# Kernel optimization log

Hardware: AMD Instinct MI355X
Metric: run time of the kernel (lower is better)

The kernel has to match this reference:

```python
import jax, jax.numpy as jnp
import numpy as np

NHEAD, DK, DV, DMODEL, L = 8, 64, 64, 512, 32

def setup_inputs() -> dict:
    key = jax.random.key(0)
    ks = jax.random.split(key, 9)
    B, N = 4, 2048
    s = 1.0 / np.sqrt(DMODEL)
    return {
        "q": jax.random.normal(ks[0], (B, N, DMODEL), jnp.float32),
        "k": jax.random.normal(ks[1], (B, N, DMODEL), jnp.float32),
        "v": jax.random.normal(ks[2], (B, N, DMODEL), jnp.float32),
        "Wq": jax.random.normal(ks[3], (DMODEL, NHEAD * DK), jnp.float32) * s,
        "Wk": jax.random.normal(ks[4], (DMODEL, NHEAD * DK), jnp.float32) * s,
        "Wv": jax.random.normal(ks[5], (DMODEL, NHEAD * DV), jnp.float32) * s,
        "Wfc": jax.random.normal(ks[6], (NHEAD * DV, DMODEL), jnp.float32) * s,
        "ln_g": jnp.ones((DMODEL,), jnp.float32),
        "ln_b": jnp.zeros((DMODEL,), jnp.float32),
    }

def reference(q, k, v, Wq, Wk, Wv, Wfc, ln_g, ln_b):
    B, Nq, _ = q.shape
    residual = q
    # project and split heads: [B, H, N, d]
    qh = (q @ Wq).reshape(B, Nq, NHEAD, DK).transpose(0, 2, 1, 3)
    kh = (k @ Wk).reshape(B, k.shape[1], NHEAD, DK).transpose(0, 2, 1, 3)
    vh = (v @ Wv).reshape(B, v.shape[1], NHEAD, DV).transpose(0, 2, 1, 3)
    # scaled dot-product scores and softmax over keys
    attn = jnp.einsum('bhqd,bhkd->bhqk', qh / jnp.sqrt(jnp.float32(DK)), kh)
    attn = jax.nn.softmax(attn, axis=-1)
    # AWG: keep entries >= l-th largest per row, renormalize
    threshold = jax.lax.top_k(attn, L)[0][..., -1:]  # [B,H,Nq,1]
    W = jnp.where(attn >= threshold, attn, 0.0)
    W_out = W / jnp.sum(W, axis=-1, keepdims=True)
    out = jnp.einsum('bhqk,bhkd->bhqd', W_out, vh)
    out = out.transpose(0, 2, 1, 3).reshape(B, Nq, NHEAD * DV)
    out = out @ Wfc + residual
    # LayerNorm, eps=1e-6
    mu = jnp.mean(out, axis=-1, keepdims=True)
    var = jnp.var(out, axis=-1, keepdims=True)
    return (out - mu) / jnp.sqrt(var + 1e-6) * ln_g + ln_b
```

## Files before the change

### kernel.cpp

```cpp
#include <hip/hip_runtime.h>
#include <hip/hip_fp16.h>

#define BATCH 4
#define NSEQ 2048
#define DMODEL 512
#define NHEAD 8
#define HDIM 64
#define LSEL 32
#define SROWU 2056
#define MAXL 128

typedef __attribute__((ext_vector_type(8))) _Float16 f16x8;
typedef __attribute__((ext_vector_type(4))) float f32x4;

__device__ inline ushort f2h(float x) { __half h = __float2half(x); return *reinterpret_cast<ushort*>(&h); }
__device__ inline uint h2sort(ushort h) { return (h & 0x8000u) ? (uint)(h ^ 0xFFFFu) : (uint)(h | 0x8000u); }
__device__ inline float sort2f(uint su) {
    ushort hb = (su & 0x8000u) ? (ushort)(su ^ 0x8000u) : (ushort)(su ^ 0xFFFFu);
    __half th; *reinterpret_cast<ushort*>(&th) = hb;
    return __half2float(th);
}

__global__ __launch_bounds__(256) void cvtA_kernel(
    const float* __restrict__ q, const float* __restrict__ k, const float* __restrict__ v,
    ushort* __restrict__ q16, ushort* __restrict__ k16, ushort* __restrict__ v16)
{
    const int z = blockIdx.y;
    const float* src = (z == 0) ? q : (z == 1) ? k : v;
    ushort* dst = (z == 0) ? q16 : (z == 1) ? k16 : v16;
    const size_t base = (size_t)blockIdx.x * 2048 + threadIdx.x * 4;
    float4 fa = *(const float4*)(src + base);
    float4 fb = *(const float4*)(src + base + 1024);
    ushort4 ha = {f2h(fa.x), f2h(fa.y), f2h(fa.z), f2h(fa.w)};
    ushort4 hb = {f2h(fb.x), f2h(fb.y), f2h(fb.z), f2h(fb.w)};
    *(ushort4*)(dst + base) = ha;
    *(ushort4*)(dst + base + 1024) = hb;
}

__global__ __launch_bounds__(256) void cvtW_kernel(
    const float* __restrict__ Wq, const float* __restrict__ Wk,
    const float* __restrict__ Wv, const float* __restrict__ Wfc,
    ushort* __restrict__ Wt)
{
    const int z = blockIdx.y;
    const float* W = (z == 0) ? Wq : (z == 1) ? Wk : (z == 2) ? Wv : Wfc;
    ushort* O = Wt + (size_t)z * DMODEL * DMODEL;
    const int gt = blockIdx.x * 256 + threadIdx.x;
    const int n = gt & 511;
    const int kc = (gt >> 9) * 16;
    uint pk[8];
#pragma unroll
    for (int i = 0; i < 8; ++i) {
        uint lo = f2h(W[(size_t)(kc + 2 * i) * DMODEL + n]);
        uint hi = f2h(W[(size_t)(kc + 2 * i + 1) * DMODEL + n]);
        pk[i] = lo | (hi << 16);
    }
    uint4 u0 = {pk[0], pk[1], pk[2], pk[3]};
    uint4 u1 = {pk[4], pk[5], pk[6], pk[7]};
    *(uint4*)(O + (size_t)n * DMODEL + kc) = u0;
    *(uint4*)(O + (size_t)n * DMODEL + kc + 8) = u1;
}

template<int MODE>
__global__ __launch_bounds__(256, 2) void hgemm_kernel(
    const ushort* __restrict__ A0, const ushort* __restrict__ A1, const ushort* __restrict__ A2,
    const ushort* __restrict__ Wt,
    ushort* __restrict__ O0, ushort* __restrict__ O1, ushort* __restrict__ O2,
    float* __restrict__ Ofc)
{
    __shared__ ushort Ah[64][40];
    __shared__ ushort Bh[512][40];

    const int tid = threadIdx.x;
    const int wave = tid >> 6, lane = tid & 63;
    const int lr = lane & 15, lg = lane >> 4;
    const int bm = blockIdx.x * 64;
    const int z = blockIdx.y;

    const ushort* A16 = (MODE == 0) ? (z == 0 ? A0 : z == 1 ? A1 : A2) : A0;
    const ushort* Wz = Wt + (size_t)((MODE == 0) ? z : 3) * (DMODEL * DMODEL);

    f32x4 acc[4][8];
#pragma unroll
    for (int i = 0; i < 4; ++i)
#pragma unroll
        for (int j = 0; j < 8; ++j) acc[i][j] = (f32x4){0.f, 0.f, 0.f, 0.f};

    const int sar = tid >> 2, sak = (tid & 3) * 8;

    for (int k0 = 0; k0 < DMODEL; k0 += 32) {
        __syncthreads();
        *(uint4*)&Ah[sar][sak] = *(const uint4*)(A16 + (size_t)(bm + sar) * DMODEL + k0 + sak);
#pragma unroll
        for (int i = 0; i < 8; ++i) {
            int n = sar + 64 * i;
            *(uint4*)&Bh[n][sak] = *(const uint4*)(Wz + (size_t)n * DMODEL + k0 + sak);
        }
        __syncthreads();
        f16x8 af[4];
#pragma unroll
        for (int fr = 0; fr < 4; ++fr) af[fr] = *(const f16x8*)&Ah[fr * 16 + lr][lg * 8];
#pragma unroll
        for (int fc2 = 0; fc2 < 8; ++fc2) {
            f16x8 bf = *(const f16x8*)&Bh[wave * 128 + fc2 * 16 + lr][lg * 8];
#pragma unroll
            for (int fr = 0; fr < 4; ++fr)
                acc[fr][fc2] = __builtin_amdgcn_mfma_f32_16x16x32_f16(af[fr], bf, acc[fr][fc2], 0, 0, 0);
        }
    }

    if (MODE == 1) {
#pragma unroll
        for (int fr = 0; fr < 4; ++fr)
#pragma unroll
            for (int fc2 = 0; fc2 < 8; ++fc2)
#pragma unroll
                for (int r = 0; r < 4; ++r)
                    Ofc[(size_t)(bm + fr * 16 + lg * 4 + r) * DMODEL + wave * 128 + fc2 * 16 + lr] = acc[fr][fc2][r];
        return;
    }

    ushort* O = (z == 0) ? O0 : (z == 1) ? O1 : O2;
    const int b = bm >> 11;
    const int nseq0 = bm & (NSEQ - 1);
    ushort* smw = (ushort*)&Bh[0][0] + wave * (64 * 72);
#pragma unroll
    for (int hp = 0; hp < 2; ++hp) {
        __syncthreads();
#pragma unroll
        for (int f4 = 0; f4 < 4; ++f4) {
            int fc2 = hp * 4 + f4;
            int nl = f4 * 16 + lr;
#pragma unroll
            for (int fr = 0; fr < 4; ++fr)
#pragma unroll
                for (int r = 0; r < 4; ++r)
                    smw[(fr * 16 + lg * 4 + r) * 72 + nl] = f2h(acc[fr][fc2][r]);
        }
        __syncthreads();
        const int h = wave * 2 + hp;
        ushort* obase = O + ((size_t)(b * NHEAD + h) * NSEQ + nseq0) * HDIM;
#pragma unroll
        for (int i = 0; i < 8; ++i) {
            int m = i * 8 + (lane >> 3);
            int dc = (lane & 7) * 8;
            *(uint4*)(obase + (size_t)m * HDIM + dc) = *(const uint4*)(smw + m * 72 + dc);
        }
    }
}

__device__ inline int wave_sum6(int c) {
    int tot = (int)__popcll(__ballot(c & 1));
    tot += (int)__popcll(__ballot(c & 2)) << 1;
    tot += (int)__popcll(__ballot(c & 4)) << 2;
    tot += (int)__popcll(__ballot(c & 8)) << 3;
    tot += (int)__popcll(__ballot(c & 16)) << 4;
    tot += (int)__popcll(__ballot(c & 32)) << 5;
    return tot;
}

__device__ uint full_thr(const ushort* Sr, int lane, uint lo0) {
    uint flo = lo0, fhi = 0xFFFFu;
    for (int it2 = 0; it2 < 16; ++it2) {
        uint mid = (flo + fhi + 1) >> 1, M = mid << 16;
        int cl = 0;
#pragma unroll
        for (int it = 0; it < 4; ++it) {
            uint4 r4 = *(const uint4*)(Sr + it * 512 + lane * 8);
            cl += ((r4.x << 16) >= M) + ((r4.x & 0xFFFF0000u) >= M);
            cl += ((r4.y << 16) >= M) + ((r4.y & 0xFFFF0000u) >= M);
            cl += ((r4.z << 16) >= M) + ((r4.z & 0xFFFF0000u) >= M);
            cl += ((r4.w << 16) >= M) + ((r4.w & 0xFFFF0000u) >= M);
        }
        bool ge = wave_sum6(cl) >= LSEL;
        flo = ge ? mid : flo;
        fhi = ge ? fhi : mid - 1;
    }
    return flo;
}

__device__ int recount(const ushort* Sr, int lane, uint th) {
    int cs = 0;
#pragma unroll
    for (int it = 0; it < 4; ++it) {
        uint4 r4 = *(const uint4*)(Sr + it * 512 + lane * 8);
        cs += ((r4.x << 16) >= th) + ((r4.x & 0xFFFF0000u) >= th);
        cs += ((r4.y << 16) >= th) + ((r4.y & 0xFFFF0000u) >= th);
        cs += ((r4.z << 16) >= th) + ((r4.z & 0xFFFF0000u) >= th);
        cs += ((r4.w << 16) >= th) + ((r4.w & 0xFFFF0000u) >= th);
    }
    return cs;
}

__device__ float extract_row(const ushort* Sr, int lane, uint th, float Mv,
                             int csel, int pre, ushort* li, float* lwp,
                             uint t0, uint t1, uint t2, uint t3)
{
    const float L2E = 1.4426950408889634f;
    float wp = 0.f;
    bool big = __any(csel > 4);
    if (!big) {
        uint tt0 = t0, tt1 = t1, tt2 = t2, tt3 = t3;
#pragma unroll
        for (int i = 0; i < 4; ++i) {
            uint t = (i == 0) ? tt0 : (i == 1) ? tt1 : (i == 2) ? tt2 : tt3;
            if (t >= th) {
                int pos = pre + i;
                float w = exp2f((sort2f(t >> 16) - Mv) * L2E);
                if (pos < MAXL) { li[pos] = (ushort)(t & 0xFFFFu); lwp[pos] = w; wp += w; }
            }
        }
    } else {
        int pos = pre;
#pragma unroll
        for (int it = 0; it < 4; ++it) {
            uint4 r4 = *(const uint4*)(Sr + it * 512 + lane * 8);
            uint ib = (uint)(it * 512 + lane * 8);
            uint wds[4] = {r4.x, r4.y, r4.z, r4.w};
#pragma unroll
            for (int c = 0; c < 4; ++c) {
                uint vL = wds[c] << 16, vH = wds[c] & 0xFFFF0000u;
                if (vL >= th) {
                    float w = exp2f((sort2f(vL >> 16) - Mv) * L2E);
                    if (pos < MAXL) { li[pos] = (ushort)(ib + c * 2); lwp[pos] = w; wp += w; }
                    ++pos;
                }
                if (vH >= th) {
                    float w = exp2f((sort2f(vH >> 16) - Mv) * L2E);
                    if (pos < MAXL) { li[pos] = (ushort)(ib + c * 2 + 1); lwp[pos] = w; wp += w; }
                    ++pos;
                }
            }
        }
    }
#pragma unroll
    for (int off = 32; off >= 1; off >>= 1) wp += __shfl_xor(wp, off);
    return wp;
}

#define INS(T0, T1, T2, T3, P) { uint m1_ = min(P, T0); T0 = max(P, T0); \
    uint m2_ = min(m1_, T1); T1 = max(m1_, T1); \
    uint m3_ = min(m2_, T2); T2 = max(m2_, T2); T3 = max(m3_, T3); }

__global__ __launch_bounds__(512, 4) void attn_kernel(
    const ushort* __restrict__ qh, const ushort* __restrict__ kh,
    const ushort* __restrict__ vh, ushort* __restrict__ ao)
{
    __shared__ __align__(16) ushort Sbuf[16 * SROWU];
    __shared__ ushort lidx[16][MAXL];
    __shared__ float  lw[16][MAXL];

    const int tid = threadIdx.x;
    const int wave = tid >> 6;
    const int lane = tid & 63;
    const int bh = blockIdx.y;
    const int q0 = blockIdx.x * 16;
    const int lr = lane & 15;
    const int lg = lane >> 4;

    const ushort* Qb = qh + ((size_t)bh * NSEQ + q0) * HDIM;
    const ushort* Kb = kh + (size_t)bh * NSEQ * HDIM;

    f16x8 qf0 = *(const f16x8*)(Qb + lr * HDIM + lg * 8);
    f16x8 qf1 = *(const f16x8*)(Qb + lr * HDIM + 32 + lg * 8);

    for (int t = 0; t < 16; ++t) {
        const int k0 = wave * 256 + t * 16;
        const ushort* Kt = Kb + (size_t)k0 * HDIM;
        f16x8 a0 = *(const f16x8*)(Kt + lr * HDIM + lg * 8);
        f16x8 a1 = *(const f16x8*)(Kt + lr * HDIM + 32 + lg * 8);
        f32x4 acc = {0.f, 0.f, 0.f, 0.f};
        acc = __builtin_amdgcn_mfma_f32_16x16x32_f16(a0, qf0, acc, 0, 0, 0);
        acc = __builtin_amdgcn_mfma_f32_16x16x32_f16(a1, qf1, acc, 0, 0, 0);
        uint2 pk;
        pk.x = h2sort(f2h(acc[0] * 0.125f)) | (h2sort(f2h(acc[1] * 0.125f)) << 16);
        pk.y = h2sort(f2h(acc[2] * 0.125f)) | (h2sort(f2h(acc[3] * 0.125f)) << 16);
        *(uint2*)&Sbuf[lr * SROWU + k0 + lg * 4] = pk;
    }
    __syncthreads();

    const __half* Vb = (const __half*)vh + (size_t)bh * NSEQ * HDIM;
    const int b = bh >> 3, hh = bh & 7;
    const unsigned long long below = (1ULL << lane) - 1ULL;

    const int qrA = wave * 2, qrB = qrA + 1;
    const ushort* SrA = &Sbuf[qrA * SROWU];
    const ushort* SrB = &Sbuf[qrB * SROWU];

    uint tA0 = 0, tA1 = 0, tA2 = 0, tA3 = 0;
    uint tB0 = 0, tB1 = 0, tB2 = 0, tB3 = 0;
#pragma unroll
    for (int it = 0; it < 4; ++it) {
        uint4 a4 = *(const uint4*)(SrA + it * 512 + lane * 8);
        uint4 b4 = *(const uint4*)(SrB + it * 512 + lane * 8);
        uint ib = (uint)(it * 512 + lane * 8);
        uint p;
        p = (a4.x << 16) | (ib + 0); INS(tA0, tA1, tA2, tA3, p);
        p = (a4.x & 0xFFFF0000u) | (ib + 1); INS(tA0, tA1, tA2, tA3, p);
        p = (a4.y << 16) | (ib + 2); INS(tA0, tA1, tA2, tA3, p);
        p = (a4.y & 0xFFFF0000u) | (ib + 3); INS(tA0, tA1, tA2, tA3, p);
        p = (a4.z << 16) | (ib + 4); INS(tA0, tA1, tA2, tA3, p);
        p = (a4.z & 0xFFFF0000u) | (ib + 5); INS(tA0, tA1, tA2, tA3, p);
        p = (a4.w << 16) | (ib + 6); INS(tA0, tA1, tA2, tA3, p);
        p = (a4.w & 0xFFFF0000u) | (ib + 7); INS(tA0, tA1, tA2, tA3, p);
        p = (b4.x << 16) | (ib + 0); INS(tB0, tB1, tB2, tB3, p);
        p = (b4.x & 0xFFFF0000u) | (ib + 1); INS(tB0, tB1, tB2, tB3, p);
        p = (b4.y << 16) | (ib + 2); INS(tB0, tB1, tB2, tB3, p);
        p = (b4.y & 0xFFFF0000u) | (ib + 3); INS(tB0, tB1, tB2, tB3, p);
        p = (b4.z << 16) | (ib + 4); INS(tB0, tB1, tB2, tB3, p);
        p = (b4.z & 0xFFFF0000u) | (ib + 5); INS(tB0, tB1, tB2, tB3, p);
        p = (b4.w << 16) | (ib + 6); INS(tB0, tB1, tB2, tB3, p);
        p = (b4.w & 0xFFFF0000u) | (ib + 7); INS(tB0, tB1, tB2, tB3, p);
    }

    uint mxA = tA0, mxB = tB0;
#pragma unroll
    for (int off = 32; off >= 1; off >>= 1) {
        mxA = max(mxA, (uint)__shfl_xor((int)mxA, off));
        mxB = max(mxB, (uint)__shfl_xor((int)mxB, off));
    }
    const float MvA = sort2f(mxA >> 16), MvB = sort2f(mxB >> 16);

    uint loA = 0, hiA = 0xFFFFu, loB = 0, hiB = 0xFFFFu;
#pragma unroll
    for (int it = 0; it < 16; ++it) {
        uint midA = (loA + hiA + 1) >> 1, MA = midA << 16;
        uint midB = (loB + hiB + 1) >> 1, MB = midB << 16;
        int cA = (tA0 >= MA) + (tA1 >= MA) + (tA2 >= MA) + (tA3 >= MA);
        int cB = (tB0 >= MB) + (tB1 >= MB) + (tB2 >= MB) + (tB3 >= MB);
        int totA = (int)__popcll(__ballot(cA & 1)) + ((int)__popcll(__ballot(cA & 2)) << 1)
                 + ((int)__popcll(__ballot(cA & 4)) << 2);
        int totB = (int)__popcll(__ballot(cB & 1)) + ((int)__popcll(__ballot(cB & 2)) << 1)
                 + ((int)__popcll(__ballot(cB & 4)) << 2);
        bool geA = totA >= LSEL, geB = totB >= LSEL;
        loA = geA ? midA : loA; hiA = geA ? hiA : midA - 1;
        loB = geB ? midB : loB; hiB = geB ? hiB : midB - 1;
    }

    uint thA = loA << 16, thB = loB << 16;
    int cgtA = 0, cselA = 0, cgtB = 0, cselB = 0;
#pragma unroll
    for (int it = 0; it < 4; ++it) {
        uint4 a4 = *(const uint4*)(SrA + it * 512 + lane * 8);
        uint4 b4 = *(const uint4*)(SrB + it * 512 + lane * 8);
#define VC(w, th, cgt, csel) { uint vL_ = (w) << 16, vH_ = (w) & 0xFFFF0000u; \
        cgt += (vL_ > th) + (vH_ > th); csel += (vL_ >= th) + (vH_ >= th); }
        VC(a4.x, thA, cgtA, cselA) VC(a4.y, thA, cgtA, cselA)
        VC(a4.z, thA, cgtA, cselA) VC(a4.w, thA, cgtA, cselA)
        VC(b4.x, thB, cgtB, cselB) VC(b4.y, thB, cgtB, cselB)
        VC(b4.z, thB, cgtB, cselB) VC(b4.w, thB, cgtB, cselB)
#undef VC
    }
    const int CgtA = wave_sum6(cgtA);
    const int CgtB = wave_sum6(cgtB);

    if (CgtA >= LSEL) {
        thA = full_thr(SrA, lane, loA) << 16;
        cselA = recount(SrA, lane, thA);
    }
    if (CgtB >= LSEL) {
        thB = full_thr(SrB, lane, loB) << 16;
        cselB = recount(SrB, lane, thB);
    }

    int preA = 0, totA2 = 0, preB = 0, totB2 = 0;
#pragma unroll
    for (int bb = 0; bb < 6; ++bb) {
        unsigned long long mA = __ballot((cselA >> bb) & 1);
        unsigned long long mB = __ballot((cselB >> bb) & 1);
        preA += (int)__popcll(mA & below) << bb; totA2 += (int)__popcll(mA) << bb;
        preB += (int)__popcll(mB & below) << bb; totB2 += (int)__popcll(mB) << bb;
    }

    float wsumA = extract_row(SrA, lane, thA, MvA, cselA, preA, &lidx[qrA][0], &lw[qrA][0], tA0, tA1, tA2, tA3);
    float wsumB = extract_row(SrB, lane, thB, MvB, cselB, preB, &lidx[qrB][0], &lw[qrB][0], tB0, tB1, tB2, tB3);

    asm volatile("s_waitcnt lgkmcnt(0)" ::: "memory");

    const int nkA = (totA2 < MAXL) ? totA2 : MAXL;
    const int nkB = (totB2 < MAXL) ? totB2 : MAXL;

    float oA = 0.f, oB = 0.f;
    {
        int j = 0;
        for (; j + 4 <= nkA; j += 4) {
            int i0 = lidx[qrA][j + 0]; float w0 = lw[qrA][j + 0];
            int i1 = lidx[qrA][j + 1]; float w1 = lw[qrA][j + 1];
            int i2 = lidx[qrA][j + 2]; float w2 = lw[qrA][j + 2];
            int i3 = lidx[qrA][j + 3]; float w3 = lw[qrA][j + 3];
            oA += w0 * __half2float(Vb[(size_t)i0 * HDIM + lane]);
            oA += w1 * __half2float(Vb[(size_t)i1 * HDIM + lane]);
            oA += w2 * __half2float(Vb[(size_t)i2 * HDIM + lane]);
            oA += w3 * __half2float(Vb[(size_t)i3 * HDIM + lane]);
        }
        for (; j < nkA; ++j)
            oA += lw[qrA][j] * __half2float(Vb[(size_t)lidx[qrA][j] * HDIM + lane]);
    }
    {
        int j = 0;
        for (; j + 4 <= nkB; j += 4) {
            int i0 = lidx[qrB][j + 0]; float w0 = lw[qrB][j + 0];
            int i1 = lidx[qrB][j + 1]; float w1 = lw[qrB][j + 1];
            int i2 = lidx[qrB][j + 2]; float w2 = lw[qrB][j + 2];
            int i3 = lidx[qrB][j + 3]; float w3 = lw[qrB][j + 3];
            oB += w0 * __half2float(Vb[(size_t)i0 * HDIM + lane]);
            oB += w1 * __half2float(Vb[(size_t)i1 * HDIM + lane]);
            oB += w2 * __half2float(Vb[(size_t)i2 * HDIM + lane]);
            oB += w3 * __half2float(Vb[(size_t)i3 * HDIM + lane]);
        }
        for (; j < nkB; ++j)
            oB += lw[qrB][j] * __half2float(Vb[(size_t)lidx[qrB][j] * HDIM + lane]);
    }

    ao[((size_t)(b * NSEQ) + q0 + qrA) * DMODEL + hh * HDIM + lane] = f2h(oA / wsumA);
    ao[((size_t)(b * NSEQ) + q0 + qrB) * DMODEL + hh * HDIM + lane] = f2h(oB / wsumB);
}

__global__ __launch_bounds__(256) void ln_kernel(
    const float* __restrict__ fcr, const float* __restrict__ resid,
    const float* __restrict__ g, const float* __restrict__ bta, float* __restrict__ out)
{
    const int row = blockIdx.x * 4 + (threadIdx.x >> 6);
    const int lane = threadIdx.x & 63;
    const size_t base = (size_t)row * DMODEL + lane * 8;
    float4 xa = *(const float4*)(fcr + base);
    float4 xb = *(const float4*)(fcr + base + 4);
    float4 ra = *(const float4*)(resid + base);
    float4 rb = *(const float4*)(resid + base + 4);
    xa.x += ra.x; xa.y += ra.y; xa.z += ra.z; xa.w += ra.w;
    xb.x += rb.x; xb.y += rb.y; xb.z += rb.z; xb.w += rb.w;
    float sum = xa.x + xa.y + xa.z + xa.w + xb.x + xb.y + xb.z + xb.w;
    float sq = xa.x * xa.x + xa.y * xa.y + xa.z * xa.z + xa.w * xa.w
             + xb.x * xb.x + xb.y * xb.y + xb.z * xb.z + xb.w * xb.w;
#pragma unroll
    for (int off = 32; off >= 1; off >>= 1) {
        sum += __shfl_xor(sum, off);
        sq += __shfl_xor(sq, off);
    }
    float mean = sum * (1.f / 512.f);
    float var = sq * (1.f / 512.f) - mean * mean;
    float rstd = rsqrtf(var + 1e-6f);
    float4 ga = *(const float4*)(g + lane * 8);
    float4 gb = *(const float4*)(g + lane * 8 + 4);
    float4 ba = *(const float4*)(bta + lane * 8);
    float4 bb = *(const float4*)(bta + lane * 8 + 4);
    float4 oa, ob;
    oa.x = (xa.x - mean) * rstd * ga.x + ba.x;
    oa.y = (xa.y - mean) * rstd * ga.y + ba.y;
    oa.z = (xa.z - mean) * rstd * ga.z + ba.z;
    oa.w = (xa.w - mean) * rstd * ga.w + ba.w;
    ob.x = (xb.x - mean) * rstd * gb.x + bb.x;
    ob.y = (xb.y - mean) * rstd * gb.y + bb.y;
    ob.z = (xb.z - mean) * rstd * gb.z + bb.z;
    ob.w = (xb.w - mean) * rstd * gb.w + bb.w;
    *(float4*)(out + base) = oa;
    *(float4*)(out + base + 4) = ob;
}

extern "C" void kernel_launch(void* const* d_in, const int* in_sizes, int n_in,
                              void* d_out, int out_size, void* d_ws, size_t ws_size,
                              hipStream_t stream)
{
    (void)in_sizes; (void)n_in; (void)out_size; (void)ws_size;

    const float* q   = (const float*)d_in[0];
    const float* k   = (const float*)d_in[1];
    const float* v   = (const float*)d_in[2];
    const float* Wq  = (const float*)d_in[3];
    const float* Wk  = (const float*)d_in[4];
    const float* Wv  = (const float*)d_in[5];
    const float* Wfc = (const float*)d_in[6];
    const float* g   = (const float*)d_in[7];
    const float* b   = (const float*)d_in[8];
    float* out = (float*)d_out;

    const size_t SZ = (size_t)BATCH * NSEQ * DMODEL;
    const size_t WSZ = (size_t)DMODEL * DMODEL;
    ushort* w16 = (ushort*)d_ws;
    ushort* q16 = w16;
    ushort* k16 = w16 + SZ;
    ushort* v16 = w16 + 2 * SZ;
    ushort* Wt  = w16 + 3 * SZ;
    ushort* qh  = Wt + 4 * WSZ;
    ushort* kh  = qh + SZ;
    ushort* vh  = kh + SZ;
    ushort* ao  = vh + SZ;
    float* fc_raw = (float*)d_ws;

    cvtA_kernel<<<dim3(2048, 3), 256, 0, stream>>>(q, k, v, q16, k16, v16);
    cvtW_kernel<<<dim3(64, 4), 256, 0, stream>>>(Wq, Wk, Wv, Wfc, Wt);
    hgemm_kernel<0><<<dim3(128, 3), 256, 0, stream>>>(q16, k16, v16, Wt, qh, kh, vh, nullptr);
    attn_kernel<<<dim3(NSEQ / 16, BATCH * NHEAD), 512, 0, stream>>>(qh, kh, vh, ao);
    hgemm_kernel<1><<<dim3(128, 1), 256, 0, stream>>>(ao, nullptr, nullptr, Wt, nullptr, nullptr, nullptr, fc_raw);
    ln_kernel<<<(BATCH * NSEQ) / 4, 256, 0, stream>>>(fc_raw, q, g, b, out);
}
```

Before: 318.0 us.

## Fuse activation fp16 conversion into projection GEMM and rework top-k selection and PV gather

```diff
diff --git a/kernel.cpp b/kernel.cpp
--- a/kernel.cpp
+++ b/kernel.cpp
@@ -21,22 +21,6 @@
     return __half2float(th);
 }
 
-__global__ __launch_bounds__(256) void cvtA_kernel(
-    const float* __restrict__ q, const float* __restrict__ k, const float* __restrict__ v,
-    ushort* __restrict__ q16, ushort* __restrict__ k16, ushort* __restrict__ v16)
-{
-    const int z = blockIdx.y;
-    const float* src = (z == 0) ? q : (z == 1) ? k : v;
-    ushort* dst = (z == 0) ? q16 : (z == 1) ? k16 : v16;
-    const size_t base = (size_t)blockIdx.x * 2048 + threadIdx.x * 4;
-    float4 fa = *(const float4*)(src + base);
-    float4 fb = *(const float4*)(src + base + 1024);
-    ushort4 ha = {f2h(fa.x), f2h(fa.y), f2h(fa.z), f2h(fa.w)};
-    ushort4 hb = {f2h(fb.x), f2h(fb.y), f2h(fb.z), f2h(fb.w)};
-    *(ushort4*)(dst + base) = ha;
-    *(ushort4*)(dst + base + 1024) = hb;
-}
-
 __global__ __launch_bounds__(256) void cvtW_kernel(
     const float* __restrict__ Wq, const float* __restrict__ Wk,
     const float* __restrict__ Wv, const float* __restrict__ Wfc,
@@ -63,7 +47,8 @@
 
 template<int MODE>
 __global__ __launch_bounds__(256, 2) void hgemm_kernel(
-    const ushort* __restrict__ A0, const ushort* __restrict__ A1, const ushort* __restrict__ A2,
+    const float* __restrict__ Fq, const float* __restrict__ Fk, const float* __restrict__ Fv,
+    const ushort* __restrict__ A16,
     const ushort* __restrict__ Wt,
     ushort* __restrict__ O0, ushort* __restrict__ O1, ushort* __restrict__ O2,
     float* __restrict__ Ofc)
@@ -77,7 +62,7 @@
     const int bm = blockIdx.x * 64;
     const int z = blockIdx.y;
 
-    const ushort* A16 = (MODE == 0) ? (z == 0 ? A0 : z == 1 ? A1 : A2) : A0;
+    const float* Af = (MODE == 0) ? (z == 0 ? Fq : z == 1 ? Fk : Fv) : nullptr;
     const ushort* Wz = Wt + (size_t)((MODE == 0) ? z : 3) * (DMODEL * DMODEL);
 
     f32x4 acc[4][8];
@@ -90,7 +75,18 @@
 
     for (int k0 = 0; k0 < DMODEL; k0 += 32) {
         __syncthreads();
-        *(uint4*)&Ah[sar][sak] = *(const uint4*)(A16 + (size_t)(bm + sar) * DMODEL + k0 + sak);
+        if (MODE == 0) {
+            float4 fa = *(const float4*)(Af + (size_t)(bm + sar) * DMODEL + k0 + sak);
+            float4 fb = *(const float4*)(Af + (size_t)(bm + sar) * DMODEL + k0 + sak + 4);
+            uint4 pk;
+            pk.x = (uint)f2h(fa.x) | ((uint)f2h(fa.y) << 16);
+            pk.y = (uint)f2h(fa.z) | ((uint)f2h(fa.w) << 16);
+            pk.z = (uint)f2h(fb.x) | ((uint)f2h(fb.y) << 16);
+            pk.w = (uint)f2h(fb.z) | ((uint)f2h(fb.w) << 16);
+            *(uint4*)&Ah[sar][sak] = pk;
+        } else {
+            *(uint4*)&Ah[sar][sak] = *(const uint4*)(A16 + (size_t)(bm + sar) * DMODEL + k0 + sak);
+        }
 #pragma unroll
         for (int i = 0; i < 8; ++i) {
             int n = sar + 64 * i;
@@ -161,6 +157,7 @@
 
 __device__ uint full_thr(const ushort* Sr, int lane, uint lo0) {
     uint flo = lo0, fhi = 0xFFFFu;
+#pragma unroll 1
     for (int it2 = 0; it2 < 16; ++it2) {
         uint mid = (flo + fhi + 1) >> 1, M = mid << 16;
         int cl = 0;
@@ -192,44 +189,29 @@
     return cs;
 }
 
-__device__ float extract_row(const ushort* Sr, int lane, uint th, float Mv,
-                             int csel, int pre, ushort* li, float* lwp,
-                             uint t0, uint t1, uint t2, uint t3)
+__device__ float extract_big(const ushort* Sr, int lane, uint th, float Mv,
+                             int pre, ushort* li, float* lwp)
 {
     const float L2E = 1.4426950408889634f;
     float wp = 0.f;
-    bool big = __any(csel > 4);
-    if (!big) {
-        uint tt0 = t0, tt1 = t1, tt2 = t2, tt3 = t3;
-#pragma unroll
-        for (int i = 0; i < 4; ++i) {
-            uint t = (i == 0) ? tt0 : (i == 1) ? tt1 : (i == 2) ? tt2 : tt3;
-            if (t >= th) {
-                int pos = pre + i;
-                float w = exp2f((sort2f(t >> 16) - Mv) * L2E);
-                if (pos < MAXL) { li[pos] = (ushort)(t & 0xFFFFu); lwp[pos] = w; wp += w; }
+    int pos = pre;
+#pragma unroll
+    for (int it = 0; it < 4; ++it) {
+        uint4 r4 = *(const uint4*)(Sr + it * 512 + lane * 8);
+        uint ib = (uint)(it * 512 + lane * 8);
+        uint wds[4] = {r4.x, r4.y, r4.z, r4.w};
+#pragma unroll
+        for (int c = 0; c < 4; ++c) {
+            uint vL = wds[c] << 16, vH = wds[c] & 0xFFFF0000u;
+            if (vL >= th) {
+                float w = exp2f((sort2f(vL >> 16) - Mv) * L2E);
+                if (pos < MAXL) { li[pos] = (ushort)(ib + c * 2); lwp[pos] = w; wp += w; }
+                ++pos;
             }
-        }
-    } else {
-        int pos = pre;
-#pragma unroll
-        for (int it = 0; it < 4; ++it) {
-            uint4 r4 = *(const uint4*)(Sr + it * 512 + lane * 8);
-            uint ib = (uint)(it * 512 + lane * 8);
-            uint wds[4] = {r4.x, r4.y, r4.z, r4.w};
-#pragma unroll
-            for (int c = 0; c < 4; ++c) {
-                uint vL = wds[c] << 16, vH = wds[c] & 0xFFFF0000u;
-                if (vL >= th) {
-                    float w = exp2f((sort2f(vL >> 16) - Mv) * L2E);
-                    if (pos < MAXL) { li[pos] = (ushort)(ib + c * 2); lwp[pos] = w; wp += w; }
-                    ++pos;
-                }
-                if (vH >= th) {
-                    float w = exp2f((sort2f(vH >> 16) - Mv) * L2E);
-                    if (pos < MAXL) { li[pos] = (ushort)(ib + c * 2 + 1); lwp[pos] = w; wp += w; }
-                    ++pos;
-                }
+            if (vH >= th) {
+                float w = exp2f((sort2f(vH >> 16) - Mv) * L2E);
+                if (pos < MAXL) { li[pos] = (ushort)(ib + c * 2 + 1); lwp[pos] = w; wp += w; }
+                ++pos;
             }
         }
     }
@@ -238,9 +220,31 @@
     return wp;
 }
 
-#define INS(T0, T1, T2, T3, P) { uint m1_ = min(P, T0); T0 = max(P, T0); \
+__device__ float extract_fast(uint t0, uint t1, uint t2, uint t3,
+                              uint th, float Mv, int pre, ushort* li, float* lwp)
+{
+    const float L2E = 1.4426950408889634f;
+    float wp = 0.f;
+    uint tt[4] = {t0, t1, t2, t3};
+#pragma unroll
+    for (int i = 0; i < 4; ++i) {
+        if (tt[i] >= th) {
+            int pos = pre + i;
+            float w = exp2f((sort2f(tt[i] >> 16) - Mv) * L2E);
+            if (pos < MAXL) { li[pos] = (ushort)(tt[i] & 0xFFFFu); lwp[pos] = w; wp += w; }
+        }
+    }
+#pragma unroll
+    for (int off = 32; off >= 1; off >>= 1) wp += __shfl_xor(wp, off);
+    return wp;
+}
+
+#define INS5(T0, T1, T2, T3, T4, P) { \
+    uint m1_ = min(P, T0); T0 = max(P, T0); \
     uint m2_ = min(m1_, T1); T1 = max(m1_, T1); \
-    uint m3_ = min(m2_, T2); T2 = max(m2_, T2); T3 = max(m3_, T3); }
+    uint m3_ = min(m2_, T2); T2 = max(m2_, T2); \
+    uint m4_ = min(m3_, T3); T3 = max(m3_, T3); \
+    T4 = max(m4_, T4); }
 
 __global__ __launch_bounds__(512, 4) void attn_kernel(
     const ushort* __restrict__ qh, const ushort* __restrict__ kh,
@@ -279,7 +283,7 @@
     }
     __syncthreads();
 
-    const __half* Vb = (const __half*)vh + (size_t)bh * NSEQ * HDIM;
+    const ushort* Vb = vh + (size_t)bh * NSEQ * HDIM;
     const int b = bh >> 3, hh = bh & 7;
     const unsigned long long below = (1ULL << lane) - 1ULL;
 
@@ -287,33 +291,33 @@
     const ushort* SrA = &Sbuf[qrA * SROWU];
     const ushort* SrB = &Sbuf[qrB * SROWU];
 
-    uint tA0 = 0, tA1 = 0, tA2 = 0, tA3 = 0;
-    uint tB0 = 0, tB1 = 0, tB2 = 0, tB3 = 0;
+    uint a0 = 0, a1 = 0, a2 = 0, a3 = 0, a4 = 0;
+    uint b0 = 0, b1 = 0, b2 = 0, b3 = 0, b4 = 0;
 #pragma unroll
     for (int it = 0; it < 4; ++it) {
-        uint4 a4 = *(const uint4*)(SrA + it * 512 + lane * 8);
-        uint4 b4 = *(const uint4*)(SrB + it * 512 + lane * 8);
+        uint4 ra = *(const uint4*)(SrA + it * 512 + lane * 8);
+        uint4 rb = *(const uint4*)(SrB + it * 512 + lane * 8);
         uint ib = (uint)(it * 512 + lane * 8);
         uint p;
-        p = (a4.x << 16) | (ib + 0); INS(tA0, tA1, tA2, tA3, p);
-        p = (a4.x & 0xFFFF0000u) | (ib + 1); INS(tA0, tA1, tA2, tA3, p);
-        p = (a4.y << 16) | (ib + 2); INS(tA0, tA1, tA2, tA3, p);
-        p = (a4.y & 0xFFFF0000u) | (ib + 3); INS(tA0, tA1, tA2, tA3, p);
-        p = (a4.z << 16) | (ib + 4); INS(tA0, tA1, tA2, tA3, p);
-        p = (a4.z & 0xFFFF0000u) | (ib + 5); INS(tA0, tA1, tA2, tA3, p);
-        p = (a4.w << 16) | (ib + 6); INS(tA0, tA1, tA2, tA3, p);
-        p = (a4.w & 0xFFFF0000u) | (ib + 7); INS(tA0, tA1, tA2, tA3, p);
-        p = (b4.x << 16) | (ib + 0); INS(tB0, tB1, tB2, tB3, p);
-        p = (b4.x & 0xFFFF0000u) | (ib + 1); INS(tB0, tB1, tB2, tB3, p);
-        p = (b4.y << 16) | (ib + 2); INS(tB0, tB1, tB2, tB3, p);
-        p = (b4.y & 0xFFFF0000u) | (ib + 3); INS(tB0, tB1, tB2, tB3, p);
-        p = (b4.z << 16) | (ib + 4); INS(tB0, tB1, tB2, tB3, p);
-        p = (b4.z & 0xFFFF0000u) | (ib + 5); INS(tB0, tB1, tB2, tB3, p);
-        p = (b4.w << 16) | (ib + 6); INS(tB0, tB1, tB2, tB3, p);
-        p = (b4.w & 0xFFFF0000u) | (ib + 7); INS(tB0, tB1, tB2, tB3, p);
-    }
-
-    uint mxA = tA0, mxB = tB0;
+        p = (ra.x << 16) | (ib + 0); INS5(a0, a1, a2, a3, a4, p);
+        p = (ra.x & 0xFFFF0000u) | (ib + 1); INS5(a0, a1, a2, a3, a4, p);
+        p = (ra.y << 16) | (ib + 2); INS5(a0, a1, a2, a3, a4, p);
+        p = (ra.y & 0xFFFF0000u) | (ib + 3); INS5(a0, a1, a2, a3, a4, p);
+        p = (ra.z << 16) | (ib + 4); INS5(a0, a1, a2, a3, a4, p);
+        p = (ra.z & 0xFFFF0000u) | (ib + 5); INS5(a0, a1, a2, a3, a4, p);
+        p = (ra.w << 16) | (ib + 6); INS5(a0, a1, a2, a3, a4, p);
+        p = (ra.w & 0xFFFF0000u) | (ib + 7); INS5(a0, a1, a2, a3, a4, p);
+        p = (rb.x << 16) | (ib + 0); INS5(b0, b1, b2, b3, b4, p);
+        p = (rb.x & 0xFFFF0000u) | (ib + 1); INS5(b0, b1, b2, b3, b4, p);
+        p = (rb.y << 16) | (ib + 2); INS5(b0, b1, b2, b3, b4, p);
+        p = (rb.y & 0xFFFF0000u) | (ib + 3); INS5(b0, b1, b2, b3, b4, p);
+        p = (rb.z << 16) | (ib + 4); INS5(b0, b1, b2, b3, b4, p);
+        p = (rb.z & 0xFFFF0000u) | (ib + 5); INS5(b0, b1, b2, b3, b4, p);
+        p = (rb.w << 16) | (ib + 6); INS5(b0, b1, b2, b3, b4, p);
+        p = (rb.w & 0xFFFF0000u) | (ib + 7); INS5(b0, b1, b2, b3, b4, p);
+    }
+
+    uint mxA = a0, mxB = b0;
 #pragma unroll
     for (int off = 32; off >= 1; off >>= 1) {
         mxA = max(mxA, (uint)__shfl_xor((int)mxA, off));
@@ -326,8 +330,8 @@
     for (int it = 0; it < 16; ++it) {
         uint midA = (loA + hiA + 1) >> 1, MA = midA << 16;
         uint midB = (loB + hiB + 1) >> 1, MB = midB << 16;
-        int cA = (tA0 >= MA) + (tA1 >= MA) + (tA2 >= MA) + (tA3 >= MA);
-        int cB = (tB0 >= MB) + (tB1 >= MB) + (tB2 >= MB) + (tB3 >= MB);
+        int cA = (a0 >= MA) + (a1 >= MA) + (a2 >= MA) + (a3 >= MA);
+        int cB = (b0 >= MB) + (b1 >= MB) + (b2 >= MB) + (b3 >= MB);
         int totA = (int)__popcll(__ballot(cA & 1)) + ((int)__popcll(__ballot(cA & 2)) << 1)
                  + ((int)__popcll(__ballot(cA & 4)) << 2);
         int totB = (int)__popcll(__ballot(cB & 1)) + ((int)__popcll(__ballot(cB & 2)) << 1)
@@ -338,28 +342,23 @@
     }
 
     uint thA = loA << 16, thB = loB << 16;
-    int cgtA = 0, cselA = 0, cgtB = 0, cselB = 0;
-#pragma unroll
-    for (int it = 0; it < 4; ++it) {
-        uint4 a4 = *(const uint4*)(SrA + it * 512 + lane * 8);
-        uint4 b4 = *(const uint4*)(SrB + it * 512 + lane * 8);
-#define VC(w, th, cgt, csel) { uint vL_ = (w) << 16, vH_ = (w) & 0xFFFF0000u; \
-        cgt += (vL_ > th) + (vH_ > th); csel += (vL_ >= th) + (vH_ >= th); }
-        VC(a4.x, thA, cgtA, cselA) VC(a4.y, thA, cgtA, cselA)
-        VC(a4.z, thA, cgtA, cselA) VC(a4.w, thA, cgtA, cselA)
-        VC(b4.x, thB, cgtB, cselB) VC(b4.y, thB, cgtB, cselB)
-        VC(b4.z, thB, cgtB, cselB) VC(b4.w, thB, cgtB, cselB)
-#undef VC
-    }
-    const int CgtA = wave_sum6(cgtA);
-    const int CgtB = wave_sum6(cgtB);
-
-    if (CgtA >= LSEL) {
-        thA = full_thr(SrA, lane, loA) << 16;
+
+    const bool missA = __any(a4 >= thA);
+    const bool missB = __any(b4 >= thB);
+
+    int cselA, cselB;
+    if (!missA) {
+        cselA = (a0 >= thA) + (a1 >= thA) + (a2 >= thA) + (a3 >= thA);
+    } else {
+        int cgt = recount(SrA, lane, thA + 0x10000u);
+        if (wave_sum6(cgt) >= LSEL) { loA = full_thr(SrA, lane, loA); thA = loA << 16; }
         cselA = recount(SrA, lane, thA);
     }
-    if (CgtB >= LSEL) {
-        thB = full_thr(SrB, lane, loB) << 16;
+    if (!missB) {
+        cselB = (b0 >= thB) + (b1 >= thB) + (b2 >= thB) + (b3 >= thB);
+    } else {
+        int cgt = recount(SrB, lane, thB + 0x10000u);
+        if (wave_sum6(cgt) >= LSEL) { loB = full_thr(SrB, lane, loB); thB = loB << 16; }
         cselB = recount(SrB, lane, thB);
     }
 
@@ -372,48 +371,46 @@
         preB += (int)__popcll(mB & below) << bb; totB2 += (int)__popcll(mB) << bb;
     }
 
-    float wsumA = extract_row(SrA, lane, thA, MvA, cselA, preA, &lidx[qrA][0], &lw[qrA][0], tA0, tA1, tA2, tA3);
-    float wsumB = extract_row(SrB, lane, thB, MvB, cselB, preB, &lidx[qrB][0], &lw[qrB][0], tB0, tB1, tB2, tB3);
-
-    asm volatile("s_waitcnt lgkmcnt(0)" ::: "memory");
+    const float wsumA = missA
+        ? extract_big(SrA, lane, thA, MvA, preA, &lidx[qrA][0], &lw[qrA][0])
+        : extract_fast(a0, a1, a2, a3, thA, MvA, preA, &lidx[qrA][0], &lw[qrA][0]);
+    const float wsumB = missB
+        ? extract_big(SrB, lane, thB, MvB, preB, &lidx[qrB][0], &lw[qrB][0])
+        : extract_fast(b0, b1, b2, b3, thB, MvB, preB, &lidx[qrB][0], &lw[qrB][0]);
 
     const int nkA = (totA2 < MAXL) ? totA2 : MAXL;
     const int nkB = (totB2 < MAXL) ? totB2 : MAXL;
 
-    float oA = 0.f, oB = 0.f;
-    {
-        int j = 0;
-        for (; j + 4 <= nkA; j += 4) {
-            int i0 = lidx[qrA][j + 0]; float w0 = lw[qrA][j + 0];
-            int i1 = lidx[qrA][j + 1]; float w1 = lw[qrA][j + 1];
-            int i2 = lidx[qrA][j + 2]; float w2 = lw[qrA][j + 2];
-            int i3 = lidx[qrA][j + 3]; float w3 = lw[qrA][j + 3];
-            oA += w0 * __half2float(Vb[(size_t)i0 * HDIM + lane]);
-            oA += w1 * __half2float(Vb[(size_t)i1 * HDIM + lane]);
-            oA += w2 * __half2float(Vb[(size_t)i2 * HDIM + lane]);
-            oA += w3 * __half2float(Vb[(size_t)i3 * HDIM + lane]);
-        }
-        for (; j < nkA; ++j)
-            oA += lw[qrA][j] * __half2float(Vb[(size_t)lidx[qrA][j] * HDIM + lane]);
-    }
-    {
-        int j = 0;
-        for (; j + 4 <= nkB; j += 4) {
-            int i0 = lidx[qrB][j + 0]; float w0 = lw[qrB][j + 0];
-            int i1 = lidx[qrB][j + 1]; float w1 = lw[qrB][j + 1];
-            int i2 = lidx[qrB][j + 2]; float w2 = lw[qrB][j + 2];
-            int i3 = lidx[qrB][j + 3]; float w3 = lw[qrB][j + 3];
-            oB += w0 * __half2float(Vb[(size_t)i0 * HDIM + lane]);
-            oB += w1 * __half2float(Vb[(size_t)i1 * HDIM + lane]);
-            oB += w2 * __half2float(Vb[(size_t)i2 * HDIM + lane]);
-            oB += w3 * __half2float(Vb[(size_t)i3 * HDIM + lane]);
-        }
-        for (; j < nkB; ++j)
-            oB += lw[qrB][j] * __half2float(Vb[(size_t)lidx[qrB][j] * HDIM + lane]);
-    }
-
-    ao[((size_t)(b * NSEQ) + q0 + qrA) * DMODEL + hh * HDIM + lane] = f2h(oA / wsumA);
-    ao[((size_t)(b * NSEQ) + q0 + qrB) * DMODEL + hh * HDIM + lane] = f2h(oB / wsumB);
+    const int half = lane >> 5;
+    const int dp = lane & 31;
+    const int qrMy = qrA + half;
+    const int nkMy = half ? nkB : nkA;
+    const float wsMy = half ? wsumB : wsumA;
+    const __half2* V2 = reinterpret_cast<const __half2*>(Vb);
+
+    float ox = 0.f, oy = 0.f;
+    int j = 0;
+    for (; j + 4 <= nkMy; j += 4) {
+        int i0 = lidx[qrMy][j + 0]; float w0 = lw[qrMy][j + 0];
+        int i1 = lidx[qrMy][j + 1]; float w1 = lw[qrMy][j + 1];
+        int i2 = lidx[qrMy][j + 2]; float w2 = lw[qrMy][j + 2];
+        int i3 = lidx[qrMy][j + 3]; float w3 = lw[qrMy][j + 3];
+        float2 v0 = __half22float2(V2[(size_t)i0 * 32 + dp]);
+        float2 v1 = __half22float2(V2[(size_t)i1 * 32 + dp]);
+        float2 v2 = __half22float2(V2[(size_t)i2 * 32 + dp]);
+        float2 v3 = __half22float2(V2[(size_t)i3 * 32 + dp]);
+        ox += w0 * v0.x + w1 * v1.x + w2 * v2.x + w3 * v3.x;
+        oy += w0 * v0.y + w1 * v1.y + w2 * v2.y + w3 * v3.y;
+    }
+    for (; j < nkMy; ++j) {
+        int i0 = lidx[qrMy][j]; float w0 = lw[qrMy][j];
+        float2 v0 = __half22float2(V2[(size_t)i0 * 32 + dp]);
+        ox += w0 * v0.x; oy += w0 * v0.y;
+    }
+
+    const float inv = 1.f / wsMy;
+    uint opk = (uint)f2h(ox * inv) | ((uint)f2h(oy * inv) << 16);
+    *(uint*)(ao + ((size_t)(b * NSEQ) + q0 + qrMy) * DMODEL + hh * HDIM + dp * 2) = opk;
 }
 
 __global__ __launch_bounds__(256) void ln_kernel(
@@ -476,21 +473,16 @@
 
     const size_t SZ = (size_t)BATCH * NSEQ * DMODEL;
     const size_t WSZ = (size_t)DMODEL * DMODEL;
-    ushort* w16 = (ushort*)d_ws;
-    ushort* q16 = w16;
-    ushort* k16 = w16 + SZ;
-    ushort* v16 = w16 + 2 * SZ;
-    ushort* Wt  = w16 + 3 * SZ;
-    ushort* qh  = Wt + 4 * WSZ;
-    ushort* kh  = qh + SZ;
-    ushort* vh  = kh + SZ;
-    ushort* ao  = vh + SZ;
-    float* fc_raw = (float*)d_ws;
-
-    cvtA_kernel<<<dim3(2048, 3), 256, 0, stream>>>(q, k, v, q16, k16, v16);
+    ushort* Wt = (ushort*)d_ws;
+    ushort* qh = Wt + 4 * WSZ;
+    ushort* kh = qh + SZ;
+    ushort* vh = kh + SZ;
+    ushort* ao = vh + SZ;
+    float* fc_raw = (float*)qh;
+
     cvtW_kernel<<<dim3(64, 4), 256, 0, stream>>>(Wq, Wk, Wv, Wfc, Wt);
-    hgemm_kernel<0><<<dim3(128, 3), 256, 0, stream>>>(q16, k16, v16, Wt, qh, kh, vh, nullptr);
+    hgemm_kernel<0><<<dim3(128, 3), 256, 0, stream>>>(q, k, v, nullptr, Wt, qh, kh, vh, nullptr);
     attn_kernel<<<dim3(NSEQ / 16, BATCH * NHEAD), 512, 0, stream>>>(qh, kh, vh, ao);
-    hgemm_kernel<1><<<dim3(128, 1), 256, 0, stream>>>(ao, nullptr, nullptr, Wt, nullptr, nullptr, nullptr, fc_raw);
+    hgemm_kernel<1><<<dim3(128, 1), 256, 0, stream>>>(nullptr, nullptr, nullptr, ao, Wt, nullptr, nullptr, nullptr, fc_raw);
     ln_kernel<<<(BATCH * NSEQ) / 4, 256, 0, stream>>>(fc_raw, q, g, b, out);
 }
```

Result: slower. 333.0 us (+4.7%).
